# Kernel optimization log

Measured on AMD Instinct MI355X. Metric: run time of the kernel, lower is better.

The kernel has to match this reference:

```python
import jax, jax.numpy as jnp
import numpy as np

NEG_SLOPE = 0.2  # PyG GATConv default leaky_relu slope
EPS = 1e-16


def setup_inputs() -> dict:
    key = jax.random.key(0)
    ks = jax.random.split(key, 8)
    N, E, F = 50000, 1600000, 128
    L, H, C = 3, 4, 32  # layers, heads, per-head channels; H*C == F
    Dh = 32             # MLP hidden (== hidden_channels)
    x = jax.random.normal(ks[0], (N, F), jnp.float32)
    edge_index = jax.random.randint(ks[1], (2, E), 0, N, jnp.int32)
    W = jax.random.normal(ks[2], (L, F, H * C), jnp.float32) * 0.1
    att_src = jax.random.normal(ks[3], (L, H, C), jnp.float32) * 0.1
    att_dst = jax.random.normal(ks[4], (L, H, C), jnp.float32) * 0.1
    b_conv = jnp.zeros((L, H * C), jnp.float32)
    W1 = jax.random.normal(ks[5], (F + H * C, Dh), jnp.float32) * 0.1
    b1 = jnp.zeros((Dh,), jnp.float32)
    W2 = jax.random.normal(ks[6], (Dh, 1), jnp.float32) * 0.1
    b2 = jnp.zeros((1,), jnp.float32)
    return {"x": x, "edge_index": edge_index, "W": W, "att_src": att_src,
            "att_dst": att_dst, "b_conv": b_conv, "W1": W1, "b1": b1,
            "W2": W2, "b2": b2}


def _gat_layer(x, src, dst, W, a_s, a_d, b, N):
    H, C = a_s.shape
    h = (x @ W).reshape(N, H, C)                      # [N,H,C]
    alpha_s = jnp.sum(h * a_s, axis=-1)               # [N,H]
    alpha_d = jnp.sum(h * a_d, axis=-1)               # [N,H]
    e = jax.nn.leaky_relu(alpha_s[src] + alpha_d[dst], NEG_SLOPE)  # [E,H]
    # segment softmax over incoming edges of each dst node
    m = jax.ops.segment_max(e, dst, num_segments=N)
    ex = jnp.exp(e - m[dst])
    s = jax.ops.segment_sum(ex, dst, num_segments=N)
    a = ex / (s[dst] + EPS)                           # [E,H]
    out = jax.ops.segment_sum(h[src] * a[:, :, None], dst, num_segments=N)
    return out.reshape(N, H * C) + b


def reference(x, edge_index, W, att_src, att_dst, b_conv, W1, b1, W2, b2):
    N = x.shape[0]
    loops = jnp.arange(N, dtype=edge_index.dtype)
    src = jnp.concatenate([edge_index[0], loops])  # PyG GATConv adds self loops
    dst = jnp.concatenate([edge_index[1], loops])
    x0 = x
    for l in range(W.shape[0]):
        x = _gat_layer(x, src, dst, W[l], att_src[l], att_dst[l], b_conv[l], N)
    h = jnp.concatenate([x, x0], axis=-1)
    h = jax.nn.relu(h @ W1 + b1)
    return jax.nn.sigmoid(h @ W2 + b2)
```

## Files before the change

### kernel.cpp

```cpp
#include <hip/hip_runtime.h>

#define NEG_SLOPE 0.2f
#define EPSF 1e-16f
#define SEG_SHIFT 13

typedef unsigned int uint;
typedef unsigned short ushort;
typedef __attribute__((ext_vector_type(8))) short short8;
typedef __attribute__((ext_vector_type(4))) float floatx4;
typedef __attribute__((ext_vector_type(4))) uint uintx4;

static __device__ __forceinline__ ushort f2bf(float f) {
    uint u = __float_as_uint(f);
    return (ushort)((u + 0x7FFFu + ((u >> 16) & 1u)) >> 16);
}
static __device__ __forceinline__ uint pack2(float a, float b) {
    return (uint)f2bf(a) | ((uint)f2bf(b) << 16);
}
static __device__ __forceinline__ float bf_lo(uint p) { return __uint_as_float(p << 16); }
static __device__ __forceinline__ float bf_hi(uint p) { return __uint_as_float(p & 0xFFFF0000u); }
static __device__ __forceinline__ short8 u2s8(uint4 v) {
    union { uint4 u; short8 s; } c; c.u = v; return c.s;
}
static __device__ __forceinline__ void load_lds16(const void* g, void* l) {
    __builtin_amdgcn_global_load_lds(
        (const __attribute__((address_space(1))) void*)g,
        (__attribute__((address_space(3))) void*)l, 16, 0, 0);
}

#define GA_LDS_BYTES (2048 * 16 + 16 * 65 * 16)

static __device__ __forceinline__ void gemm_body(
    char* smraw, const uint4* __restrict__ xb, const uint4* __restrict__ Wp,
    const float* __restrict__ att_s, const float* __restrict__ att_d,
    uint* __restrict__ h2, float* __restrict__ alpha_s,
    float* __restrict__ alpha_d, int N, int rowBase)
{
    uint4* sW = (uint4*)smraw;
    uint4* sX = sW + 2048;

    const int t = threadIdx.x;
    const int wb = t & ~63;

#pragma unroll
    for (int i = 0; i < 8; ++i)
        load_lds16(Wp + i * 256 + t, sW + i * 256 + wb);

#pragma unroll
    for (int i = 0; i < 4; ++i) {
        int f = t + i * 256;
        int row = f >> 4, c8 = f & 15;
        uint4 v = make_uint4(0u, 0u, 0u, 0u);
        if (rowBase + row < N) v = xb[(size_t)(rowBase + row) * 16 + c8];
        sX[c8 * 65 + row] = v;
    }
    __syncthreads();

    const int w = t >> 6, lane = t & 63, q = lane >> 4, l15 = lane & 15;
    short8 xf[4];
#pragma unroll
    for (int s = 0; s < 4; ++s)
        xf[s] = u2s8(sX[(4 * s + q) * 65 + 16 * w + l15]);

    floatx4 acc[8];
#pragma unroll
    for (int ct = 0; ct < 8; ++ct) acc[ct] = (floatx4){0.f, 0.f, 0.f, 0.f};
#pragma unroll
    for (int ct = 0; ct < 8; ++ct) {
#pragma unroll
        for (int s = 0; s < 4; ++s) {
            short8 wf = u2s8(sW[(4 * s + q) * 128 + 16 * ct + l15]);
            acc[ct] = __builtin_amdgcn_mfma_f32_16x16x32_bf16(wf, xf[s], acc[ct], 0, 0, 0);
        }
    }

    const int node = rowBase + 16 * w + l15;
    if (node < N) {
        uint2* hp = (uint2*)(h2 + (size_t)node * 64);
#pragma unroll
        for (int ct = 0; ct < 8; ++ct) {
            uint2 o;
            o.x = pack2(acc[ct][0], acc[ct][1]);
            o.y = pack2(acc[ct][2], acc[ct][3]);
            hp[4 * ct + q] = o;
        }
    }
    float ps[4], pd[4];
#pragma unroll
    for (int hd = 0; hd < 4; ++hd) {
        const float4 as0 = *(const float4*)(att_s + 32 * hd + 4 * q);
        const float4 as1 = *(const float4*)(att_s + 32 * hd + 16 + 4 * q);
        const float4 ad0 = *(const float4*)(att_d + 32 * hd + 4 * q);
        const float4 ad1 = *(const float4*)(att_d + 32 * hd + 16 + 4 * q);
        floatx4 c0 = acc[2 * hd], c1 = acc[2 * hd + 1];
        ps[hd] = c0[0] * as0.x + c0[1] * as0.y + c0[2] * as0.z + c0[3] * as0.w
               + c1[0] * as1.x + c1[1] * as1.y + c1[2] * as1.z + c1[3] * as1.w;
        pd[hd] = c0[0] * ad0.x + c0[1] * ad0.y + c0[2] * ad0.z + c0[3] * ad0.w
               + c1[0] * ad1.x + c1[1] * ad1.y + c1[2] * ad1.z + c1[3] * ad1.w;
    }
#pragma unroll
    for (int hd = 0; hd < 4; ++hd) {
        ps[hd] += __shfl_xor(ps[hd], 16);
        ps[hd] += __shfl_xor(ps[hd], 32);
        pd[hd] += __shfl_xor(pd[hd], 16);
        pd[hd] += __shfl_xor(pd[hd], 32);
    }
    if (node < N) {
        alpha_s[(size_t)node * 4 + q] = ps[q];
        alpha_d[(size_t)node * 4 + q] = pd[q];
    }
}

__global__ __launch_bounds__(256) void prep_count_kernel(
    const float* __restrict__ W, const float* __restrict__ W1,
    const float* __restrict__ x, uint4* __restrict__ Wp,
    uint4* __restrict__ W1p, uint4* __restrict__ xb,
    const int* __restrict__ ei, int E, int NB,
    int* __restrict__ bucket_count, int L, int N, int nbPrep)
{
    __shared__ int cnt[256];
    if ((int)blockIdx.x >= nbPrep) {
        cnt[threadIdx.x] = 0;
        __syncthreads();
        const int base = (blockIdx.x - nbPrep) * 2048 + threadIdx.x;
#pragma unroll
        for (int j = 0; j < 8; ++j) {
            int idx = base + j * 256;
            if (idx < E) atomicAdd(&cnt[ei[E + idx] >> 8], 1);
        }
        __syncthreads();
        int c = cnt[threadIdx.x];
        if ((int)threadIdx.x < NB && c) atomicAdd(&bucket_count[threadIdx.x], c);
        return;
    }
    int id = blockIdx.x * 256 + threadIdx.x;
    const int nW = L * 2048;
    const int nX = N * 16;
    if (id < nW) {
        int l = id >> 11, s = id & 2047;
        int chunk = s >> 7, col = s & 127;
        const float* wp = W + (size_t)l * 16384 + (chunk * 8) * 128 + col;
        uint4 pk;
        pk.x = pack2(wp[0],   wp[128]);
        pk.y = pack2(wp[256], wp[384]);
        pk.z = pack2(wp[512], wp[640]);
        pk.w = pack2(wp[768], wp[896]);
        Wp[id] = pk;
    } else if (id < nW + 1024) {
        int s = id - nW;
        int chunk = s >> 5, col = s & 31;
        const float* wp = W1 + (chunk * 8) * 32 + col;
        uint4 pk;
        pk.x = pack2(wp[0],   wp[32]);
        pk.y = pack2(wp[64],  wp[96]);
        pk.z = pack2(wp[128], wp[160]);
        pk.w = pack2(wp[192], wp[224]);
        W1p[s] = pk;
    } else if (id < nW + 1024 + nX) {
        int xid = id - nW - 1024;
        int row = xid >> 4, c8 = xid & 15;
        const float4* xp = (const float4*)(x + (size_t)row * 128 + c8 * 8);
        float4 v0 = xp[0], v1 = xp[1];
        uint4 pk;
        pk.x = pack2(v0.x, v0.y); pk.y = pack2(v0.z, v0.w);
        pk.z = pack2(v1.x, v1.y); pk.w = pack2(v1.z, v1.w);
        xb[xid] = pk;
    }
}

__global__ __launch_bounds__(256) void dist_gemm_kernel(
    const int* __restrict__ ei, int E, int NB,
    const int* __restrict__ bucket_count, int* __restrict__ bucket_cursor,
    uint* __restrict__ bdata, int nbEd,
    const uint4* __restrict__ xb, const uint4* __restrict__ Wp,
    const float* __restrict__ att_s, const float* __restrict__ att_d,
    uint* __restrict__ h2, float* __restrict__ alpha_s,
    float* __restrict__ alpha_d, int N)
{
    __shared__ __align__(16) char smraw[GA_LDS_BYTES];
    const int t = threadIdx.x;
    if ((int)blockIdx.x >= nbEd) {
        gemm_body(smraw, xb, Wp, att_s, att_d, h2, alpha_s, alpha_d, N,
                  (blockIdx.x - nbEd) * 64);
        return;
    }
    int* cnt = (int*)smraw;
    int* sc  = cnt + 256;
    int* bb  = sc + 256;
    cnt[t] = 0;
    __syncthreads();
    const int base = blockIdx.x * 2048 + t;
    int srcs[8], dsts[8], rank[8];
#pragma unroll
    for (int j = 0; j < 8; ++j) {
        int idx = base + j * 256;
        if (idx < E) {
            srcs[j] = ei[idx];
            dsts[j] = ei[E + idx];
            rank[j] = atomicAdd(&cnt[dsts[j] >> 8], 1);
        } else dsts[j] = -1;
    }
    __syncthreads();
    int bc = (t < NB) ? bucket_count[t] : 0;
    sc[t] = bc;
    __syncthreads();
    for (int off = 1; off < 256; off <<= 1) {
        int x = sc[t];
        int a = (t >= off) ? sc[t - off] : 0;
        __syncthreads();
        sc[t] = x + a;
        __syncthreads();
    }
    int gbase = sc[t] - bc;
    int c = cnt[t];
    bb[t] = (t < NB && c) ? (gbase + atomicAdd(&bucket_cursor[t], c)) : 0;
    __syncthreads();
#pragma unroll
    for (int j = 0; j < 8; ++j) {
        if (dsts[j] >= 0) {
            int b = dsts[j] >> 8;
            bdata[bb[b] + rank[j]] = (uint)srcs[j] | ((uint)(dsts[j] & 255) << 16);
        }
    }
}

#define BCAP 12800
__global__ __launch_bounds__(256) void bucket_csr_kernel(
    const uint* __restrict__ bdata, const int* __restrict__ bucket_count,
    int NB, int E, int* __restrict__ row_start, ushort* __restrict__ csr_src,
    int N)
{
    __shared__ int hist[2048];
    __shared__ int cur[2048];
    __shared__ int scn[256];
    __shared__ int sb[256];
    __shared__ ushort buf[BCAP];
    const int b = blockIdx.x;
    const int t = threadIdx.x;

    int bc = (t < NB) ? bucket_count[t] : 0;
    sb[t] = bc;
    __syncthreads();
    for (int off = 1; off < 256; off <<= 1) {
        int x = sb[t];
        int a = (t >= off) ? sb[t - off] : 0;
        __syncthreads();
        sb[t] = x + a;
        __syncthreads();
    }
    const int beg = (b > 0) ? sb[b - 1] : 0;
    const int sz = sb[b] - beg;
    if (b == 0 && t == 0) row_start[N] = E;

#pragma unroll
    for (int j = 0; j < 8; ++j) hist[t * 8 + j] = 0;
    __syncthreads();
    for (int i = t; i < sz; i += 256) {
        uint d = bdata[beg + i];
        int key = (int)((d >> 16) << 3) | (int)((d & 0xFFFFu) >> SEG_SHIFT);
        atomicAdd(&hist[key], 1);
    }
    __syncthreads();
    int local[8]; int s = 0;
#pragma unroll
    for (int j = 0; j < 8; ++j) { local[j] = hist[t * 8 + j]; s += local[j]; }
    scn[t] = s;
    __syncthreads();
    for (int off = 1; off < 256; off <<= 1) {
        int x = scn[t];
        int a = (t >= off) ? scn[t - off] : 0;
        __syncthreads();
        scn[t] = x + a;
        __syncthreads();
    }
    int run = scn[t] - s;
#pragma unroll
    for (int j = 0; j < 8; ++j) { cur[t * 8 + j] = run; run += local[j]; }
    __syncthreads();
    int node = b * 256 + t;
    if (node < N) row_start[node] = beg + cur[t << 3];
    __syncthreads();
    if (sz <= BCAP) {
        for (int i = t; i < sz; i += 256) {
            uint d = bdata[beg + i];
            int key = (int)((d >> 16) << 3) | (int)((d & 0xFFFFu) >> SEG_SHIFT);
            int pos = atomicAdd(&cur[key], 1);
            buf[pos] = (ushort)(d & 0xFFFFu);
        }
        __syncthreads();
        for (int i = t; i < sz; i += 256) csr_src[beg + i] = buf[i];
    } else {
        for (int i = t; i < sz; i += 256) {
            uint d = bdata[beg + i];
            int key = (int)((d >> 16) << 3) | (int)((d & 0xFFFFu) >> SEG_SHIFT);
            int pos = atomicAdd(&cur[key], 1);
            csr_src[beg + pos] = (ushort)(d & 0xFFFFu);
        }
    }
}

static __device__ __forceinline__ void agg_core(
    const ushort* __restrict__ csr_src, const int* __restrict__ row_start,
    const float* __restrict__ alpha_s, const float* __restrict__ alpha_d,
    const uint* __restrict__ h2, int g, int l, int head,
    float& a0, float& a1, float& a2, float& a3,
    float& a4, float& a5, float& a6, float& a7, float& sx)
{
    const char* hbase = (const char*)h2 + (size_t)l * 16;
    const float ad = alpha_d[g * 4 + head];

    float e = alpha_s[g * 4 + head] + ad;
    e = e > 0.f ? e : NEG_SLOPE * e;
    float ex = __expf(e);
    uint4 q = *(const uint4*)(hbase + (uint)g * 256u);
    a0 = ex * bf_lo(q.x); a1 = ex * bf_hi(q.x);
    a2 = ex * bf_lo(q.y); a3 = ex * bf_hi(q.y);
    a4 = ex * bf_lo(q.z); a5 = ex * bf_hi(q.z);
    a6 = ex * bf_lo(q.w); a7 = ex * bf_hi(q.w);
    sx = ex;

    const int beg = row_start[g];
    const int end = row_start[g + 1];
    int k = beg;
    for (; k + 4 <= end; k += 4) {
        uint s0 = csr_src[k], s1 = csr_src[k + 1];
        uint s2 = csr_src[k + 2], s3 = csr_src[k + 3];
        uint4 q0 = *(const uint4*)(hbase + s0 * 256u);
        uint4 q1 = *(const uint4*)(hbase + s1 * 256u);
        uint4 q2 = *(const uint4*)(hbase + s2 * 256u);
        uint4 q3 = *(const uint4*)(hbase + s3 * 256u);
        float e0 = alpha_s[s0 * 4 + head] + ad;
        float e1 = alpha_s[s1 * 4 + head] + ad;
        float e2 = alpha_s[s2 * 4 + head] + ad;
        float e3 = alpha_s[s3 * 4 + head] + ad;
        e0 = e0 > 0.f ? e0 : NEG_SLOPE * e0;
        e1 = e1 > 0.f ? e1 : NEG_SLOPE * e1;
        e2 = e2 > 0.f ? e2 : NEG_SLOPE * e2;
        e3 = e3 > 0.f ? e3 : NEG_SLOPE * e3;
        float x0 = __expf(e0), x1 = __expf(e1);
        float x2 = __expf(e2), x3 = __expf(e3);
        a0 += x0 * bf_lo(q0.x) + x1 * bf_lo(q1.x) + x2 * bf_lo(q2.x) + x3 * bf_lo(q3.x);
        a1 += x0 * bf_hi(q0.x) + x1 * bf_hi(q1.x) + x2 * bf_hi(q2.x) + x3 * bf_hi(q3.x);
        a2 += x0 * bf_lo(q0.y) + x1 * bf_lo(q1.y) + x2 * bf_lo(q2.y) + x3 * bf_lo(q3.y);
        a3 += x0 * bf_hi(q0.y) + x1 * bf_hi(q1.y) + x2 * bf_hi(q2.y) + x3 * bf_hi(q3.y);
        a4 += x0 * bf_lo(q0.z) + x1 * bf_lo(q1.z) + x2 * bf_lo(q2.z) + x3 * bf_lo(q3.z);
        a5 += x0 * bf_hi(q0.z) + x1 * bf_hi(q1.z) + x2 * bf_hi(q2.z) + x3 * bf_hi(q3.z);
        a6 += x0 * bf_lo(q0.w) + x1 * bf_lo(q1.w) + x2 * bf_lo(q2.w) + x3 * bf_lo(q3.w);
        a7 += x0 * bf_hi(q0.w) + x1 * bf_hi(q1.w) + x2 * bf_hi(q2.w) + x3 * bf_hi(q3.w);
        sx += x0 + x1 + x2 + x3;
    }
    for (; k < end; ++k) {
        uint s0 = csr_src[k];
        float e0 = alpha_s[s0 * 4 + head] + ad;
        uint4 q0 = *(const uint4*)(hbase + s0 * 256u);
        e0 = e0 > 0.f ? e0 : NEG_SLOPE * e0;
        float x0 = __expf(e0);
        a0 += x0 * bf_lo(q0.x); a1 += x0 * bf_hi(q0.x);
        a2 += x0 * bf_lo(q0.y); a3 += x0 * bf_hi(q0.y);
        a4 += x0 * bf_lo(q0.z); a5 += x0 * bf_hi(q0.z);
        a6 += x0 * bf_lo(q0.w); a7 += x0 * bf_hi(q0.w);
        sx += x0;
    }
}

__global__ __launch_bounds__(256) void aggemm_kernel(
    const ushort* __restrict__ csr_src, const int* __restrict__ row_start,
    const float* __restrict__ alpha_s, const float* __restrict__ alpha_d,
    const uint* __restrict__ h2in, const float* __restrict__ b,
    const uint4* __restrict__ Wnext,
    const float* __restrict__ att_s, const float* __restrict__ att_d,
    uint* __restrict__ h2out, float* __restrict__ alpha_s_out,
    float* __restrict__ alpha_d_out, int N)
{
    __shared__ __align__(16) uint4 tile[16 * 17];
    const int t = threadIdx.x;
    const int nodeBase = blockIdx.x * 16;
    const int gl = t >> 4;
    const int g = nodeBase + gl;
    const int l = t & 15;
    const bool active = g < N;

    uint4 o = make_uint4(0u, 0u, 0u, 0u);
    if (active) {
        float a0, a1, a2, a3, a4, a5, a6, a7, sx;
        agg_core(csr_src, row_start, alpha_s, alpha_d, h2in, g, l, l >> 2,
                 a0, a1, a2, a3, a4, a5, a6, a7, sx);
        const float inv = 1.f / (sx + EPSF);
        const float4 b0 = ((const float4*)b)[l * 2];
        const float4 b1 = ((const float4*)b)[l * 2 + 1];
        o.x = pack2(b0.x + a0 * inv, b0.y + a1 * inv);
        o.y = pack2(b0.z + a2 * inv, b0.w + a3 * inv);
        o.z = pack2(b1.x + a4 * inv, b1.y + a5 * inv);
        o.w = pack2(b1.z + a6 * inv, b1.w + a7 * inv);
    }
    tile[gl * 17 + l] = o;
    __syncthreads();

    const int w = t >> 6, lane = t & 63, q = lane >> 4, l15 = lane & 15;
    floatx4 acc0 = (floatx4){0.f, 0.f, 0.f, 0.f};
    floatx4 acc1 = (floatx4){0.f, 0.f, 0.f, 0.f};
#pragma unroll
    for (int s = 0; s < 4; ++s) {
        short8 xfr = u2s8(tile[l15 * 17 + 4 * s + q]);
        short8 wf0 = u2s8(Wnext[(4 * s + q) * 128 + 16 * (2 * w) + l15]);
        short8 wf1 = u2s8(Wnext[(4 * s + q) * 128 + 16 * (2 * w + 1) + l15]);
        acc0 = __builtin_amdgcn_mfma_f32_16x16x32_bf16(wf0, xfr, acc0, 0, 0, 0);
        acc1 = __builtin_amdgcn_mfma_f32_16x16x32_bf16(wf1, xfr, acc1, 0, 0, 0);
    }
    const int node = nodeBase + l15;
    if (node < N) {
        uint2* hp = (uint2*)(h2out + (size_t)node * 64);
        uint2 o0, o1;
        o0.x = pack2(acc0[0], acc0[1]); o0.y = pack2(acc0[2], acc0[3]);
        o1.x = pack2(acc1[0], acc1[1]); o1.y = pack2(acc1[2], acc1[3]);
        hp[4 * (2 * w) + q] = o0;
        hp[4 * (2 * w + 1) + q] = o1;
    }
    const float4 as0 = *(const float4*)(att_s + 32 * w + 4 * q);
    const float4 as1 = *(const float4*)(att_s + 32 * w + 16 + 4 * q);
    const float4 ad0 = *(const float4*)(att_d + 32 * w + 4 * q);
    const float4 ad1 = *(const float4*)(att_d + 32 * w + 16 + 4 * q);
    float ps = acc0[0] * as0.x + acc0[1] * as0.y + acc0[2] * as0.z + acc0[3] * as0.w
             + acc1[0] * as1.x + acc1[1] * as1.y + acc1[2] * as1.z + acc1[3] * as1.w;
    float pd = acc0[0] * ad0.x + acc0[1] * ad0.y + acc0[2] * ad0.z + acc0[3] * ad0.w
             + acc1[0] * ad1.x + acc1[1] * ad1.y + acc1[2] * ad1.z + acc1[3] * ad1.w;
    ps += __shfl_xor(ps, 16); ps += __shfl_xor(ps, 32);
    pd += __shfl_xor(pd, 16); pd += __shfl_xor(pd, 32);
    if (node < N && q == 0) {
        alpha_s_out[(size_t)node * 4 + w] = ps;
        alpha_d_out[(size_t)node * 4 + w] = pd;
    }
}

__global__ __launch_bounds__(256) void agg_csr_kernel(
    const ushort* __restrict__ csr_src, const int* __restrict__ row_start,
    const float* __restrict__ alpha_s, const float* __restrict__ alpha_d,
    const uint* __restrict__ h2, const float* __restrict__ b,
    uint* __restrict__ outb, int N)
{
    const int g = (blockIdx.x * 256 + threadIdx.x) >> 4;
    const int l = threadIdx.x & 15;
    if (g >= N) return;
    float a0, a1, a2, a3, a4, a5, a6, a7, sx;
    agg_core(csr_src, row_start, alpha_s, alpha_d, h2, g, l, l >> 2,
             a0, a1, a2, a3, a4, a5, a6, a7, sx);
    const float inv = 1.f / (sx + EPSF);
    const float4 b0 = ((const float4*)b)[l * 2];
    const float4 b1 = ((const float4*)b)[l * 2 + 1];
    uintx4 o;
    o.x = pack2(b0.x + a0 * inv, b0.y + a1 * inv);
    o.y = pack2(b0.z + a2 * inv, b0.w + a3 * inv);
    o.z = pack2(b1.x + a4 * inv, b1.y + a5 * inv);
    o.w = pack2(b1.z + a6 * inv, b1.w + a7 * inv);
    __builtin_nontemporal_store(o, (uintx4*)(outb + (size_t)g * 64 + l * 4));
}

__global__ __launch_bounds__(256) void mlp_kernel(
    const uint4* __restrict__ xb3, const uint4* __restrict__ xb0,
    const uint4* __restrict__ W1p, const float* __restrict__ b1,
    const float* __restrict__ W2, const float* __restrict__ b2,
    float* __restrict__ out, int N)
{
    __shared__ __align__(16) uint4 sA[32 * 65];
    __shared__ __align__(16) uint4 sB[32 * 32];
    const int t = threadIdx.x;
    const int wb = t & ~63;
    const int rowBase = blockIdx.x * 64;

#pragma unroll
    for (int i = 0; i < 4; ++i)
        load_lds16(W1p + i * 256 + t, sB + i * 256 + wb);
#pragma unroll
    for (int i = 0; i < 8; ++i) {
        int f = t + i * 256;
        int c = f & 31, row = f >> 5;
        uint4 v = make_uint4(0u, 0u, 0u, 0u);
        int grow = rowBase + row;
        if (grow < N)
            v = (c < 16) ? xb3[(size_t)grow * 16 + c]
                         : xb0[(size_t)grow * 16 + (c - 16)];
        sA[c * 65 + row] = v;
    }
    __syncthreads();

    const int w = t >> 6, lane = t & 63, q = lane >> 4, l15 = lane & 15;
    floatx4 acc0 = (floatx4){0.f, 0.f, 0.f, 0.f};
    floatx4 acc1 = (floatx4){0.f, 0.f, 0.f, 0.f};
#pragma unroll
    for (int s = 0; s < 8; ++s) {
        short8 a = u2s8(sA[(4 * s + q) * 65 + 16 * w + l15]);
        acc0 = __builtin_amdgcn_mfma_f32_16x16x32_bf16(a, u2s8(sB[(4 * s + q) * 32 + l15]), acc0, 0, 0, 0);
        acc1 = __builtin_amdgcn_mfma_f32_16x16x32_bf16(a, u2s8(sB[(4 * s + q) * 32 + 16 + l15]), acc1, 0, 0, 0);
    }
    const float b1a = b1[l15], b1b = b1[16 + l15];
    const float w2a = W2[l15], w2b = W2[16 + l15];
    const float b2v = b2[0];
#pragma unroll
    for (int r = 0; r < 4; ++r) {
        int row = rowBase + 16 * w + 4 * q + r;
        float v0 = acc0[r] + b1a; v0 = v0 > 0.f ? v0 : 0.f;
        float v1 = acc1[r] + b1b; v1 = v1 > 0.f ? v1 : 0.f;
        float p = v0 * w2a + v1 * w2b;
        p += __shfl_xor(p, 1);
        p += __shfl_xor(p, 2);
        p += __shfl_xor(p, 4);
        p += __shfl_xor(p, 8);
        if (l15 == 0 && row < N)
            out[row] = 1.f / (1.f + __expf(-(p + b2v)));
    }
}

extern "C" void kernel_launch(void* const* d_in, const int* in_sizes, int n_in,
                              void* d_out, int out_size, void* d_ws, size_t ws_size,
                              hipStream_t stream)
{
    const float* x       = (const float*)d_in[0];
    const int*   ei      = (const int*)d_in[1];
    const float* W       = (const float*)d_in[2];
    const float* att_src = (const float*)d_in[3];
    const float* att_dst = (const float*)d_in[4];
    const float* b_conv  = (const float*)d_in[5];
    const float* W1      = (const float*)d_in[6];
    const float* b1      = (const float*)d_in[7];
    const float* W2      = (const float*)d_in[8];
    const float* b2      = (const float*)d_in[9];
    float* outp = (float*)d_out;

    const int N = in_sizes[0] / 128;
    const int E = in_sizes[1] / 2;
    const int L = in_sizes[2] / (128 * 128);
    const int NB = (N + 255) >> 8;

    char* ws = (char*)d_ws;
    uint*  h2a     = (uint*)ws;
    uint*  h2b     = h2a + (size_t)N * 64;
    uint4* xb0     = (uint4*)(h2b + (size_t)N * 64);
    uint4* xb      = xb0 + (size_t)N * 16;
    float* alpha_s = (float*)(xb + (size_t)N * 16);
    float* alpha_d = alpha_s + (size_t)N * 4;
    uint4* Wp      = (uint4*)(alpha_d + (size_t)N * 4);
    uint4* W1p     = Wp + (size_t)L * 2048;
    int* bucket_count  = (int*)(W1p + 1024);
    int* bucket_cursor = bucket_count + 256;
    int* row_start     = bucket_cursor + 256;
    uint* bdata        = (uint*)(row_start + N + 1);
    ushort* csr_src    = (ushort*)(bdata + E);

    const int nbEc = (E + 2047) / 2048;
    const int nbEd = (E + 2047) / 2048;
    const int gBlocks = (N + 63) / 64;
    const int aggBlocks = (N * 16 + 255) / 256;
    const int prepItems = L * 2048 + 1024 + N * 16;
    const int nbPrep = (prepItems + 255) / 256;

    (void)hipMemsetAsync(bucket_count, 0, 512 * sizeof(int), stream);

    prep_count_kernel<<<nbPrep + nbEc, 256, 0, stream>>>(
        W, W1, x, Wp, W1p, xb0, ei, E, NB, bucket_count, L, N, nbPrep);

    dist_gemm_kernel<<<nbEd + gBlocks, 256, 0, stream>>>(
        ei, E, NB, bucket_count, bucket_cursor, bdata, nbEd,
        xb0, Wp, att_src, att_dst, h2a, alpha_s, alpha_d, N);

    bucket_csr_kernel<<<NB, 256, 0, stream>>>(bdata, bucket_count, NB, E,
                                              row_start, csr_src, N);

    uint* hin = h2a;
    uint* hout = h2b;
    for (int l = 0; l < L; ++l) {
        if (l < L - 1) {
            aggemm_kernel<<<aggBlocks, 256, 0, stream>>>(
                csr_src, row_start, alpha_s, alpha_d, hin,
                b_conv + (size_t)l * 128, Wp + (size_t)(l + 1) * 2048,
                att_src + (size_t)(l + 1) * 128, att_dst + (size_t)(l + 1) * 128,
                hout, alpha_s, alpha_d, N);
            uint* tmp = hin; hin = hout; hout = tmp;
        } else {
            agg_csr_kernel<<<aggBlocks, 256, 0, stream>>>(
                csr_src, row_start, alpha_s, alpha_d, hin,
                b_conv + (size_t)l * 128, (uint*)xb, N);
        }
    }

    mlp_kernel<<<gBlocks, 256, 0, stream>>>(
        xb, xb0, W1p, b1, W2, b2, outp, N);
}
```

Measured before the change: 340.8 us.

## Fuse final GAT aggregation with MLP head and double-buffer attention scores

Merges the last-layer aggregation and the MLP into one kernel. Each 16-node block aggregates, stages the bf16 result next to the original features in LDS, then runs the 32-wide MLP with MFMA in two waves. This removes one launch and the global write and read of the layer-3 output. The alpha arrays are now ping-ponged between two buffers instead of updated in place, and layer launches are unrolled for L=3, which drops generality for other layer counts.

```diff
diff --git a/kernel.cpp b/kernel.cpp
--- a/kernel.cpp
+++ b/kernel.cpp
@@ -432,81 +432,71 @@
     }
 }
 
-__global__ __launch_bounds__(256) void agg_csr_kernel(
+__global__ __launch_bounds__(256) void aggmlp_kernel(
     const ushort* __restrict__ csr_src, const int* __restrict__ row_start,
     const float* __restrict__ alpha_s, const float* __restrict__ alpha_d,
-    const uint* __restrict__ h2, const float* __restrict__ b,
-    uint* __restrict__ outb, int N)
-{
-    const int g = (blockIdx.x * 256 + threadIdx.x) >> 4;
-    const int l = threadIdx.x & 15;
-    if (g >= N) return;
-    float a0, a1, a2, a3, a4, a5, a6, a7, sx;
-    agg_core(csr_src, row_start, alpha_s, alpha_d, h2, g, l, l >> 2,
-             a0, a1, a2, a3, a4, a5, a6, a7, sx);
-    const float inv = 1.f / (sx + EPSF);
-    const float4 b0 = ((const float4*)b)[l * 2];
-    const float4 b1 = ((const float4*)b)[l * 2 + 1];
-    uintx4 o;
-    o.x = pack2(b0.x + a0 * inv, b0.y + a1 * inv);
-    o.y = pack2(b0.z + a2 * inv, b0.w + a3 * inv);
-    o.z = pack2(b1.x + a4 * inv, b1.y + a5 * inv);
-    o.w = pack2(b1.z + a6 * inv, b1.w + a7 * inv);
-    __builtin_nontemporal_store(o, (uintx4*)(outb + (size_t)g * 64 + l * 4));
-}
-
-__global__ __launch_bounds__(256) void mlp_kernel(
-    const uint4* __restrict__ xb3, const uint4* __restrict__ xb0,
-    const uint4* __restrict__ W1p, const float* __restrict__ b1,
-    const float* __restrict__ W2, const float* __restrict__ b2,
-    float* __restrict__ out, int N)
-{
-    __shared__ __align__(16) uint4 sA[32 * 65];
-    __shared__ __align__(16) uint4 sB[32 * 32];
+    const uint* __restrict__ h2in, const float* __restrict__ b,
+    const uint4* __restrict__ xb0, const uint4* __restrict__ W1p,
+    const float* __restrict__ b1, const float* __restrict__ W2,
+    const float* __restrict__ b2, float* __restrict__ out, int N)
+{
+    __shared__ __align__(16) uint4 tile[16 * 33];
+    __shared__ float pr[32];
     const int t = threadIdx.x;
-    const int wb = t & ~63;
-    const int rowBase = blockIdx.x * 64;
-
-#pragma unroll
-    for (int i = 0; i < 4; ++i)
-        load_lds16(W1p + i * 256 + t, sB + i * 256 + wb);
-#pragma unroll
-    for (int i = 0; i < 8; ++i) {
-        int f = t + i * 256;
-        int c = f & 31, row = f >> 5;
-        uint4 v = make_uint4(0u, 0u, 0u, 0u);
-        int grow = rowBase + row;
-        if (grow < N)
-            v = (c < 16) ? xb3[(size_t)grow * 16 + c]
-                         : xb0[(size_t)grow * 16 + (c - 16)];
-        sA[c * 65 + row] = v;
-    }
+    const int nodeBase = blockIdx.x * 16;
+    const int gl = t >> 4;
+    const int g = nodeBase + gl;
+    const int l = t & 15;
+
+    tile[gl * 33 + 16 + l] =
+        (g < N) ? xb0[(size_t)g * 16 + l] : make_uint4(0u, 0u, 0u, 0u);
+
+    uint4 o = make_uint4(0u, 0u, 0u, 0u);
+    if (g < N) {
+        float a0, a1, a2, a3, a4, a5, a6, a7, sx;
+        agg_core(csr_src, row_start, alpha_s, alpha_d, h2in, g, l, l >> 2,
+                 a0, a1, a2, a3, a4, a5, a6, a7, sx);
+        const float inv = 1.f / (sx + EPSF);
+        const float4 b0 = ((const float4*)b)[l * 2];
+        const float4 b1v = ((const float4*)b)[l * 2 + 1];
+        o.x = pack2(b0.x + a0 * inv, b0.y + a1 * inv);
+        o.y = pack2(b0.z + a2 * inv, b0.w + a3 * inv);
+        o.z = pack2(b1v.x + a4 * inv, b1v.y + a5 * inv);
+        o.w = pack2(b1v.z + a6 * inv, b1v.w + a7 * inv);
+    }
+    tile[gl * 33 + l] = o;
     __syncthreads();
 
     const int w = t >> 6, lane = t & 63, q = lane >> 4, l15 = lane & 15;
-    floatx4 acc0 = (floatx4){0.f, 0.f, 0.f, 0.f};
-    floatx4 acc1 = (floatx4){0.f, 0.f, 0.f, 0.f};
-#pragma unroll
-    for (int s = 0; s < 8; ++s) {
-        short8 a = u2s8(sA[(4 * s + q) * 65 + 16 * w + l15]);
-        acc0 = __builtin_amdgcn_mfma_f32_16x16x32_bf16(a, u2s8(sB[(4 * s + q) * 32 + l15]), acc0, 0, 0, 0);
-        acc1 = __builtin_amdgcn_mfma_f32_16x16x32_bf16(a, u2s8(sB[(4 * s + q) * 32 + 16 + l15]), acc1, 0, 0, 0);
-    }
-    const float b1a = b1[l15], b1b = b1[16 + l15];
-    const float w2a = W2[l15], w2b = W2[16 + l15];
-    const float b2v = b2[0];
-#pragma unroll
-    for (int r = 0; r < 4; ++r) {
-        int row = rowBase + 16 * w + 4 * q + r;
-        float v0 = acc0[r] + b1a; v0 = v0 > 0.f ? v0 : 0.f;
-        float v1 = acc1[r] + b1b; v1 = v1 > 0.f ? v1 : 0.f;
-        float p = v0 * w2a + v1 * w2b;
-        p += __shfl_xor(p, 1);
-        p += __shfl_xor(p, 2);
-        p += __shfl_xor(p, 4);
-        p += __shfl_xor(p, 8);
-        if (l15 == 0 && row < N)
-            out[row] = 1.f / (1.f + __expf(-(p + b2v)));
+    if (w < 2) {
+        floatx4 acc = (floatx4){0.f, 0.f, 0.f, 0.f};
+#pragma unroll
+        for (int s = 0; s < 8; ++s) {
+            short8 a = u2s8(tile[l15 * 33 + 4 * s + q]);
+            short8 bb = u2s8(W1p[(4 * s + q) * 32 + 16 * w + l15]);
+            acc = __builtin_amdgcn_mfma_f32_16x16x32_bf16(a, bb, acc, 0, 0, 0);
+        }
+        const int col = 16 * w + l15;
+        const float b1c = b1[col], w2c = W2[col];
+#pragma unroll
+        for (int r = 0; r < 4; ++r) {
+            float v = acc[r] + b1c;
+            v = v > 0.f ? v : 0.f;
+            float p = v * w2c;
+            p += __shfl_xor(p, 1);
+            p += __shfl_xor(p, 2);
+            p += __shfl_xor(p, 4);
+            p += __shfl_xor(p, 8);
+            if (l15 == 0) pr[w * 16 + 4 * q + r] = p;
+        }
+    }
+    __syncthreads();
+    if (t < 16) {
+        int node = nodeBase + t;
+        if (node < N) {
+            float z = pr[t] + pr[16 + t] + b2[0];
+            out[node] = 1.f / (1.f + __expf(-z));
+        }
     }
 }
 
@@ -532,14 +522,15 @@
     const int NB = (N + 255) >> 8;
 
     char* ws = (char*)d_ws;
-    uint*  h2a     = (uint*)ws;
-    uint*  h2b     = h2a + (size_t)N * 64;
-    uint4* xb0     = (uint4*)(h2b + (size_t)N * 64);
-    uint4* xb      = xb0 + (size_t)N * 16;
-    float* alpha_s = (float*)(xb + (size_t)N * 16);
-    float* alpha_d = alpha_s + (size_t)N * 4;
-    uint4* Wp      = (uint4*)(alpha_d + (size_t)N * 4);
-    uint4* W1p     = Wp + (size_t)L * 2048;
+    uint*  h2a      = (uint*)ws;
+    uint*  h2b      = h2a + (size_t)N * 64;
+    uint4* xb0      = (uint4*)(h2b + (size_t)N * 64);
+    float* alphaA_s = (float*)(xb0 + (size_t)N * 16);
+    float* alphaA_d = alphaA_s + (size_t)N * 4;
+    float* alphaB_s = alphaA_d + (size_t)N * 4;
+    float* alphaB_d = alphaB_s + (size_t)N * 4;
+    uint4* Wp       = (uint4*)(alphaB_d + (size_t)N * 4);
+    uint4* W1p      = Wp + (size_t)L * 2048;
     int* bucket_count  = (int*)(W1p + 1024);
     int* bucket_cursor = bucket_count + 256;
     int* row_start     = bucket_cursor + 256;
@@ -549,7 +540,7 @@
     const int nbEc = (E + 2047) / 2048;
     const int nbEd = (E + 2047) / 2048;
     const int gBlocks = (N + 63) / 64;
-    const int aggBlocks = (N * 16 + 255) / 256;
+    const int aggBlocks = (N + 15) / 16;
     const int prepItems = L * 2048 + 1024 + N * 16;
     const int nbPrep = (prepItems + 255) / 256;
 
@@ -560,28 +551,24 @@
 
     dist_gemm_kernel<<<nbEd + gBlocks, 256, 0, stream>>>(
         ei, E, NB, bucket_count, bucket_cursor, bdata, nbEd,
-        xb0, Wp, att_src, att_dst, h2a, alpha_s, alpha_d, N);
+        xb0, Wp, att_src, att_dst, h2a, alphaA_s, alphaA_d, N);
 
     bucket_csr_kernel<<<NB, 256, 0, stream>>>(bdata, bucket_count, NB, E,
                                               row_start, csr_src, N);
 
-    uint* hin = h2a;
-    uint* hout = h2b;
-    for (int l = 0; l < L; ++l) {
-        if (l < L - 1) {
-            aggemm_kernel<<<aggBlocks, 256, 0, stream>>>(
-                csr_src, row_start, alpha_s, alpha_d, hin,
-                b_conv + (size_t)l * 128, Wp + (size_t)(l + 1) * 2048,
-                att_src + (size_t)(l + 1) * 128, att_dst + (size_t)(l + 1) * 128,
-                hout, alpha_s, alpha_d, N);
-            uint* tmp = hin; hin = hout; hout = tmp;
-        } else {
-            agg_csr_kernel<<<aggBlocks, 256, 0, stream>>>(
-                csr_src, row_start, alpha_s, alpha_d, hin,
-                b_conv + (size_t)l * 128, (uint*)xb, N);
-        }
-    }
-
-    mlp_kernel<<<gBlocks, 256, 0, stream>>>(
-        xb, xb0, W1p, b1, W2, b2, outp, N);
-}
+    aggemm_kernel<<<aggBlocks, 256, 0, stream>>>(
+        csr_src, row_start, alphaA_s, alphaA_d, h2a,
+        b_conv + 0 * 128, Wp + (size_t)1 * 2048,
+        att_src + (size_t)1 * 128, att_dst + (size_t)1 * 128,
+        h2b, alphaB_s, alphaB_d, N);
+
+    aggemm_kernel<<<aggBlocks, 256, 0, stream>>>(
+        csr_src, row_start, alphaB_s, alphaB_d, h2b,
+        b_conv + (size_t)1 * 128, Wp + (size_t)2 * 2048,
+        att_src + (size_t)2 * 128, att_dst + (size_t)2 * 128,
+        h2a, alphaA_s, alphaA_d, N);
+
+    aggmlp_kernel<<<aggBlocks, 256, 0, stream>>>(
+        csr_src, row_start, alphaA_s, alphaA_d, h2a,
+        b_conv + (size_t)2 * 128, xb0, W1p, b1, W2, b2, outp, N);
+}
```

Measured after the change: 326.0 us. 1.05x faster.
